# Optimization experiments

Measured on AMD Instinct MI355X. Metric: run time of the kernel, lower is better.

The kernel has to match this reference:

```python
import jax, jax.numpy as jnp
import numpy as np

DIM = 2048
NUM_HEADS = 8
HEAD_DIM = DIM // NUM_HEADS
BATCH = 16384
EPS = 1e-5


def setup_inputs() -> dict:
    key = jax.random.key(0)
    ks = jax.random.split(key, 10)
    s = 1.0 / np.sqrt(DIM)
    inp = {
        "x": jax.random.normal(ks[0], (BATCH, 1, DIM), dtype=jnp.float32),
        "w_q": jax.random.uniform(ks[1], (DIM, DIM), jnp.float32, -s, s),
        "b_q": jax.random.uniform(ks[2], (DIM,), jnp.float32, -s, s),
        "w_k": jax.random.uniform(ks[3], (DIM, DIM), jnp.float32, -s, s),
        "b_k": jax.random.uniform(ks[4], (DIM,), jnp.float32, -s, s),
        "w_v": jax.random.uniform(ks[5], (DIM, DIM), jnp.float32, -s, s),
        "b_v": jax.random.uniform(ks[6], (DIM,), jnp.float32, -s, s),
        "w_o": jax.random.uniform(ks[7], (DIM, DIM), jnp.float32, -s, s),
        "b_o": jax.random.uniform(ks[8], (DIM,), jnp.float32, -s, s),
        "ln_gamma": jnp.ones((DIM,), jnp.float32),
        "ln_beta": jnp.zeros((DIM,), jnp.float32),
    }
    return inp


def _layer_norm(x, gamma, beta):
    mean = jnp.mean(x, axis=-1, keepdims=True)
    var = jnp.mean(jnp.square(x - mean), axis=-1, keepdims=True)
    return (x - mean) * jax.lax.rsqrt(var + EPS) * gamma + beta


def reference(x, w_q, b_q, w_k, b_k, w_v, b_v, w_o, b_o, ln_gamma, ln_beta):
    # x: (B, 1, D). Dropout is identity (eval mode).
    residual = x
    h = _layer_norm(x, ln_gamma, ln_beta)
    q = h @ w_q.T + b_q  # (B, 1, D)
    k = h @ w_k.T + b_k
    v = h @ w_v.T + b_v
    B = x.shape[0]
    # (B, H, 1, hd)
    qh = q.reshape(B, 1, NUM_HEADS, HEAD_DIM).transpose(0, 2, 1, 3)
    kh = k.reshape(B, 1, NUM_HEADS, HEAD_DIM).transpose(0, 2, 1, 3)
    vh = v.reshape(B, 1, NUM_HEADS, HEAD_DIM).transpose(0, 2, 1, 3)
    scale = HEAD_DIM ** -0.5
    # (B, H, 1, 1); with seq_len=1 softmax is trivially 1, but keep the math faithful
    scores = jnp.einsum("bhqd,bhkd->bhqk", qh, kh) * scale
    probs = jax.nn.softmax(scores, axis=-1)
    attn = jnp.einsum("bhqk,bhkd->bhqd", probs, vh)  # (B, H, 1, hd)
    attn = attn.transpose(0, 2, 1, 3).reshape(B, 1, DIM)
    out = attn @ w_o.T + b_o
    out = out + residual
    return out[:, 0, :]  # squeeze seq dim -> (B, D)
```

## Files before the change

kernel.cpp:

```cpp
#include <hip/hip_runtime.h>
#include <hip/hip_bf16.h>
#include <cstdint>

#define D_MODEL 2048
#define N_BATCH 16384

typedef __attribute__((ext_vector_type(8))) __bf16 bf16x8;
typedef __attribute__((ext_vector_type(4))) float f32x4;

__device__ __forceinline__ unsigned short f2bf(float f) {
    unsigned int u = __builtin_bit_cast(unsigned int, f);
    u += 0x7fffu + ((u >> 16) & 1u);
    return (unsigned short)(u >> 16);
}

__global__ __launch_bounds__(256) void ln_kernel(
    const float* __restrict__ x, const float* __restrict__ gamma,
    const float* __restrict__ beta, unsigned short* __restrict__ h)
{
    const int row = blockIdx.x;
    const int t = threadIdx.x;
    const float4* x4 = reinterpret_cast<const float4*>(x + (long)row * D_MODEL);
    float4 a = x4[t];
    float4 b = x4[256 + t];
    float s  = a.x + a.y + a.z + a.w + b.x + b.y + b.z + b.w;
    float ss = a.x*a.x + a.y*a.y + a.z*a.z + a.w*a.w
             + b.x*b.x + b.y*b.y + b.z*b.z + b.w*b.w;
    #pragma unroll
    for (int off = 32; off; off >>= 1) {
        s  += __shfl_xor(s, off);
        ss += __shfl_xor(ss, off);
    }
    __shared__ float red[8];
    const int lane = t & 63, wid = t >> 6;
    if (lane == 0) { red[wid*2] = s; red[wid*2+1] = ss; }
    __syncthreads();
    s  = red[0] + red[2] + red[4] + red[6];
    ss = red[1] + red[3] + red[5] + red[7];
    const float mean = s * (1.0f / D_MODEL);
    const float var  = ss * (1.0f / D_MODEL) - mean * mean;
    const float inv  = rsqrtf(var + 1e-5f);

    const float4* g4  = reinterpret_cast<const float4*>(gamma);
    const float4* be4 = reinterpret_cast<const float4*>(beta);
    ushort4* h4 = reinterpret_cast<ushort4*>(h + (long)row * D_MODEL);
    {
        float4 g = g4[t], be = be4[t];
        ushort4 o;
        o.x = f2bf((a.x - mean) * inv * g.x + be.x);
        o.y = f2bf((a.y - mean) * inv * g.y + be.y);
        o.z = f2bf((a.z - mean) * inv * g.z + be.z);
        o.w = f2bf((a.w - mean) * inv * g.w + be.w);
        h4[t] = o;
    }
    {
        float4 g = g4[256 + t], be = be4[256 + t];
        ushort4 o;
        o.x = f2bf((b.x - mean) * inv * g.x + be.x);
        o.y = f2bf((b.y - mean) * inv * g.y + be.y);
        o.z = f2bf((b.z - mean) * inv * g.z + be.z);
        o.w = f2bf((b.w - mean) * inv * g.w + be.w);
        h4[256 + t] = o;
    }
}

__global__ __launch_bounds__(256) void transpose_f32_to_bf16(
    const float* __restrict__ in, unsigned short* __restrict__ out, int Dm)
{
    __shared__ float tile[32][33];
    const int nb = Dm >> 5;
    const int k0 = (blockIdx.x % nb) * 32;
    const int j0 = (blockIdx.x / nb) * 32;
    const int tx = threadIdx.x & 31, ty0 = threadIdx.x >> 5;
    #pragma unroll
    for (int i = 0; i < 32; i += 8) {
        int j = ty0 + i;
        tile[j][tx] = in[(long)(j0 + j) * Dm + k0 + tx];
    }
    __syncthreads();
    #pragma unroll
    for (int i = 0; i < 32; i += 8) {
        int kk = ty0 + i;
        out[(long)(k0 + kk) * Dm + j0 + tx] = f2bf(tile[tx][kk]);
    }
}

__global__ __launch_bounds__(256) void convert_bf16(
    const float* __restrict__ in, unsigned short* __restrict__ out, long n)
{
    long i = ((long)blockIdx.x * 256 + threadIdx.x) * 8;
    if (i >= n) return;
    const float4* in4 = reinterpret_cast<const float4*>(in + i);
    float4 a = in4[0], b = in4[1];
    union { unsigned short u[8]; uint4 v; } o;
    o.u[0] = f2bf(a.x); o.u[1] = f2bf(a.y); o.u[2] = f2bf(a.z); o.u[3] = f2bf(a.w);
    o.u[4] = f2bf(b.x); o.u[5] = f2bf(b.y); o.u[6] = f2bf(b.z); o.u[7] = f2bf(b.w);
    *reinterpret_cast<uint4*>(out + i) = o.v;
}

__global__ __launch_bounds__(256) void bias_combine(
    const float* __restrict__ w_o, const float* __restrict__ b_v,
    const float* __restrict__ b_o, float* __restrict__ b_c)
{
    const int n = blockIdx.x;
    const int t = threadIdx.x;
    const float4* w4 = reinterpret_cast<const float4*>(w_o + (long)n * D_MODEL);
    const float4* v4 = reinterpret_cast<const float4*>(b_v);
    float4 a = w4[t], b = w4[256 + t], va = v4[t], vb = v4[256 + t];
    float s = a.x*va.x + a.y*va.y + a.z*va.z + a.w*va.w
            + b.x*vb.x + b.y*vb.y + b.z*vb.z + b.w*vb.w;
    #pragma unroll
    for (int off = 32; off; off >>= 1) s += __shfl_xor(s, off);
    __shared__ float red[4];
    const int lane = t & 63, wid = t >> 6;
    if (lane == 0) red[wid] = s;
    __syncthreads();
    if (t == 0) b_c[n] = red[0] + red[1] + red[2] + red[3] + b_o[n];
}

__global__ __launch_bounds__(256, 2) void gemm_bt_128(
    const unsigned short* __restrict__ A, const unsigned short* __restrict__ B,
    unsigned short* __restrict__ C, int M, int N, int K)
{
    const int nBN = N >> 7;
    int wg = blockIdx.x;
    const int nwg = gridDim.x;
    const int cpx = nwg >> 3;
    wg = (wg & 7) * cpx + (wg >> 3);
    const int bm = wg / nBN, bn = wg % nBN;

    const int t = threadIdx.x;
    const int lane = t & 63, wid = t >> 6;
    const int wr = wid >> 1, wc = wid & 1;

    __shared__ __align__(16) unsigned short Alds[128 * 32];
    __shared__ __align__(16) unsigned short Blds[128 * 32];

    f32x4 acc[4][4];
    #pragma unroll
    for (int i = 0; i < 4; i++)
        #pragma unroll
        for (int j = 0; j < 4; j++) acc[i][j] = (f32x4){0.f, 0.f, 0.f, 0.f};

    const long Abase = (long)bm * 128 * K;
    const long Bbase = (long)bn * 128 * K;
    const int ci0 = wid * 64 + lane;
    const int ci1 = 256 + ci0;
    const int r0 = ci0 >> 2, c0 = (ci0 & 3) * 8;
    const int r1 = ci1 >> 2, c1 = (ci1 & 3) * 8;

    const int arow = wr * 64 + (lane & 15);
    const int brow = wc * 64 + (lane & 15);
    const int koff = (lane >> 4) * 8;

    for (int k0 = 0; k0 < K; k0 += 32) {
        __builtin_amdgcn_global_load_lds(
            (const __attribute__((address_space(1))) void*)(A + Abase + (long)r0 * K + k0 + c0),
            (__attribute__((address_space(3))) void*)(Alds + wid * 512), 16, 0, 0);
        __builtin_amdgcn_global_load_lds(
            (const __attribute__((address_space(1))) void*)(A + Abase + (long)r1 * K + k0 + c1),
            (__attribute__((address_space(3))) void*)(Alds + 2048 + wid * 512), 16, 0, 0);
        __builtin_amdgcn_global_load_lds(
            (const __attribute__((address_space(1))) void*)(B + Bbase + (long)r0 * K + k0 + c0),
            (__attribute__((address_space(3))) void*)(Blds + wid * 512), 16, 0, 0);
        __builtin_amdgcn_global_load_lds(
            (const __attribute__((address_space(1))) void*)(B + Bbase + (long)r1 * K + k0 + c1),
            (__attribute__((address_space(3))) void*)(Blds + 2048 + wid * 512), 16, 0, 0);
        __syncthreads();

        bf16x8 af[4], bfr[4];
        #pragma unroll
        for (int m = 0; m < 4; m++)
            af[m] = *reinterpret_cast<const bf16x8*>(&Alds[(arow + m * 16) * 32 + koff]);
        #pragma unroll
        for (int n = 0; n < 4; n++)
            bfr[n] = *reinterpret_cast<const bf16x8*>(&Blds[(brow + n * 16) * 32 + koff]);
        #pragma unroll
        for (int m = 0; m < 4; m++)
            #pragma unroll
            for (int n = 0; n < 4; n++)
                acc[m][n] = __builtin_amdgcn_mfma_f32_16x16x32_bf16(af[m], bfr[n], acc[m][n], 0, 0, 0);
        __syncthreads();
    }

    const int crow0 = bm * 128 + wr * 64 + ((lane >> 4) << 2);
    const int ccol0 = bn * 128 + wc * 64 + (lane & 15);
    #pragma unroll
    for (int m = 0; m < 4; m++)
        #pragma unroll
        for (int j = 0; j < 4; j++) {
            const long r = crow0 + m * 16 + j;
            #pragma unroll
            for (int n = 0; n < 4; n++)
                C[r * N + ccol0 + n * 16] = f2bf(acc[m][n][j]);
        }
}

__global__ __launch_bounds__(512, 2) void gemm_bt_256(
    const unsigned short* __restrict__ A, const unsigned short* __restrict__ B,
    float* __restrict__ C, const float* __restrict__ bias,
    const float* __restrict__ resid, int M, int N, int K)
{
    __shared__ __align__(16) char lds[131072];

    const int nBN = N >> 8;
    int wg = blockIdx.x;
    const int cpx = gridDim.x >> 3;
    wg = (wg & 7) * cpx + (wg >> 3);
    const int bm = wg / nBN, bn = wg % nBN;

    const int t = threadIdx.x;
    const int lane = t & 63, wid = t >> 6;
    const int wr = wid >> 2;
    const int wcn = wid & 3;

    const int r_lo = t >> 2, cch = t & 3;
    const int schunk = (cch ^ ((r_lo >> 2) & 3)) * 8;
    const unsigned short* sA0 = A + (long)(bm * 256 + r_lo) * K + schunk;
    const unsigned short* sA1 = sA0 + (long)128 * K;
    const unsigned short* sB0 = B + (long)(bn * 256 + r_lo) * K + schunk;
    const unsigned short* sB1 = sB0 + (long)128 * K;

#define STAGE_A(d) do { \
    __builtin_amdgcn_global_load_lds((const __attribute__((address_space(1))) void*)sA0, \
        (__attribute__((address_space(3))) void*)(lds + (d) * 32768 + wid * 1024), 16, 0, 0); \
    __builtin_amdgcn_global_load_lds((const __attribute__((address_space(1))) void*)sA1, \
        (__attribute__((address_space(3))) void*)(lds + (d) * 32768 + 8192 + wid * 1024), 16, 0, 0); \
    sA0 += 32; sA1 += 32; } while (0)
#define STAGE_B(d) do { \
    __builtin_amdgcn_global_load_lds((const __attribute__((address_space(1))) void*)sB0, \
        (__attribute__((address_space(3))) void*)(lds + (d) * 32768 + 16384 + wid * 1024), 16, 0, 0); \
    __builtin_amdgcn_global_load_lds((const __attribute__((address_space(1))) void*)sB1, \
        (__attribute__((address_space(3))) void*)(lds + (d) * 32768 + 24576 + wid * 1024), 16, 0, 0); \
    sB0 += 32; sB1 += 32; } while (0)

    const int l15 = lane & 15, l4 = lane >> 4;
    const int koffb = ((l4 ^ ((l15 >> 2) & 3)) << 4);
    const int aRowB = (wr * 128 + l15) * 64 + koffb;
    const int bRowB = 16384 + (wcn * 64 + l15) * 64 + koffb;

    f32x4 acc[8][4];
    #pragma unroll
    for (int i = 0; i < 8; i++)
        #pragma unroll
        for (int j = 0; j < 4; j++) acc[i][j] = (f32x4){0.f, 0.f, 0.f, 0.f};

    const int nt = K >> 5;
    STAGE_A(0); STAGE_B(0);
    STAGE_A(1); STAGE_B(1);
    STAGE_A(2); STAGE_B(2);

    for (int kt = 0; kt < nt; ++kt) {
        const int bufb = (kt & 3) * 32768;
        const int slack = nt - 1 - kt;
        if (slack >= 2)      asm volatile("s_waitcnt vmcnt(8)" ::: "memory");
        else if (slack == 1) asm volatile("s_waitcnt vmcnt(4)" ::: "memory");
        else                 asm volatile("s_waitcnt vmcnt(0)" ::: "memory");
        __builtin_amdgcn_s_barrier();
        __builtin_amdgcn_sched_barrier(0);

        bf16x8 af[4], bfr[4];
        #pragma unroll
        for (int n = 0; n < 4; n++)
            bfr[n] = *reinterpret_cast<const bf16x8*>(lds + bufb + bRowB + n * 1024);
        #pragma unroll
        for (int m = 0; m < 4; m++)
            af[m] = *reinterpret_cast<const bf16x8*>(lds + bufb + aRowB + m * 1024);
        if (kt + 3 < nt) STAGE_A((kt + 3) & 3);
        __builtin_amdgcn_s_setprio(1);
        #pragma unroll
        for (int m = 0; m < 4; m++)
            #pragma unroll
            for (int n = 0; n < 4; n++)
                acc[m][n] = __builtin_amdgcn_mfma_f32_16x16x32_bf16(af[m], bfr[n], acc[m][n], 0, 0, 0);
        __builtin_amdgcn_s_setprio(0);

        __builtin_amdgcn_s_barrier();
        __builtin_amdgcn_sched_barrier(0);

        #pragma unroll
        for (int m = 0; m < 4; m++)
            af[m] = *reinterpret_cast<const bf16x8*>(lds + bufb + aRowB + 4096 + m * 1024);
        if (kt + 3 < nt) STAGE_B((kt + 3) & 3);
        __builtin_amdgcn_s_setprio(1);
        #pragma unroll
        for (int m = 0; m < 4; m++)
            #pragma unroll
            for (int n = 0; n < 4; n++)
                acc[4 + m][n] = __builtin_amdgcn_mfma_f32_16x16x32_bf16(af[m], bfr[n], acc[4 + m][n], 0, 0, 0);
        __builtin_amdgcn_s_setprio(0);
    }
#undef STAGE_A
#undef STAGE_B

    const int crow0 = bm * 256 + wr * 128 + l4 * 4;
    const int ccol0 = bn * 256 + wcn * 64 + l15;
    #pragma unroll
    for (int m = 0; m < 8; m++)
        #pragma unroll
        for (int j = 0; j < 4; j++) {
            const long r = crow0 + m * 16 + j;
            float* crow = C + r * N;
            const float* rrow = resid + r * N;
            #pragma unroll
            for (int n = 0; n < 4; n++) {
                const int col = ccol0 + n * 16;
                crow[col] = acc[m][n][j] + bias[col] + rrow[col];
            }
        }
}

extern "C" void kernel_launch(void* const* d_in, const int* in_sizes, int n_in,
                              void* d_out, int out_size, void* d_ws, size_t ws_size,
                              hipStream_t stream) {
    const float* x     = (const float*)d_in[0];
    const float* w_v   = (const float*)d_in[5];
    const float* b_v   = (const float*)d_in[6];
    const float* w_o   = (const float*)d_in[7];
    const float* b_o   = (const float*)d_in[8];
    const float* gamma = (const float*)d_in[9];
    const float* beta  = (const float*)d_in[10];
    float* out = (float*)d_out;

    char* ws = (char*)d_ws;
    unsigned short* h   = (unsigned short*)(ws);
    unsigned short* wvT = (unsigned short*)(ws + 67108864L);
    unsigned short* woB = (unsigned short*)(ws + 67108864L + 8388608L);
    unsigned short* Wc  = (unsigned short*)(ws + 67108864L + 2 * 8388608L);
    float*          b_c = (float*)(ws + 67108864L + 3 * 8388608L);

    ln_kernel<<<N_BATCH, 256, 0, stream>>>(x, gamma, beta, h);
    transpose_f32_to_bf16<<<(D_MODEL / 32) * (D_MODEL / 32), 256, 0, stream>>>(w_v, wvT, D_MODEL);
    convert_bf16<<<(D_MODEL * (long)D_MODEL) / (256 * 8), 256, 0, stream>>>(w_o, woB, (long)D_MODEL * D_MODEL);
    bias_combine<<<D_MODEL, 256, 0, stream>>>(w_o, b_v, b_o, b_c);
    gemm_bt_128<<<(D_MODEL / 128) * (D_MODEL / 128), 256, 0, stream>>>(
        woB, wvT, Wc, D_MODEL, D_MODEL, D_MODEL);
    gemm_bt_256<<<(N_BATCH / 256) * (D_MODEL / 256), 512, 0, stream>>>(
        h, Wc, out, b_c, x, N_BATCH, D_MODEL, D_MODEL);
}
```

Baseline: 251.2 us.

## Shrink main GEMM tile to 256x128 with triple-buffered LDS for higher occupancy

The large GEMM now uses a 256x128 output tile per 512-thread block instead of 256x256. It keeps a 3-stage LDS ring of 24 KB per stage instead of 4 stages of 32 KB, and asks for 4 blocks per CU. The per-iteration split into two barrier-separated MFMA halves is replaced by one staged load and one 16-MFMA block, with an explicit lgkmcnt wait. This doubles the grid and raises occupancy, at the cost of halving per-block reuse of A and loading it twice as often from global memory, with a shallower prefetch depth.

After: 257.7 us. 1.03x slower.

```diff
diff --git a/kernel.cpp b/kernel.cpp
--- a/kernel.cpp
+++ b/kernel.cpp
@@ -196,14 +196,14 @@
         }
 }
 
-__global__ __launch_bounds__(512, 2) void gemm_bt_256(
+__global__ __launch_bounds__(512, 4) void gemm_bt_256(
     const unsigned short* __restrict__ A, const unsigned short* __restrict__ B,
     float* __restrict__ C, const float* __restrict__ bias,
     const float* __restrict__ resid, int M, int N, int K)
 {
-    __shared__ __align__(16) char lds[131072];
-
-    const int nBN = N >> 8;
+    __shared__ __align__(16) char lds[73728];
+
+    const int nBN = N >> 7;
     int wg = blockIdx.x;
     const int cpx = gridDim.x >> 3;
     wg = (wg & 7) * cpx + (wg >> 3);
@@ -211,54 +211,53 @@
 
     const int t = threadIdx.x;
     const int lane = t & 63, wid = t >> 6;
-    const int wr = wid >> 2;
-    const int wcn = wid & 3;
+    const int wr = wid >> 1;
+    const int wcn = wid & 1;
 
     const int r_lo = t >> 2, cch = t & 3;
-    const int schunk = (cch ^ ((r_lo >> 2) & 3)) * 8;
+    const int schunk = (cch ^ ((r_lo >> 1) & 3)) * 8;
     const unsigned short* sA0 = A + (long)(bm * 256 + r_lo) * K + schunk;
     const unsigned short* sA1 = sA0 + (long)128 * K;
-    const unsigned short* sB0 = B + (long)(bn * 256 + r_lo) * K + schunk;
-    const unsigned short* sB1 = sB0 + (long)128 * K;
-
-#define STAGE_A(d) do { \
+    const unsigned short* sB0 = B + (long)(bn * 128 + r_lo) * K + schunk;
+
+#define STAGE_AB(d) do { \
+    const int dst_ = (d) * 24576 + wid * 1024; \
     __builtin_amdgcn_global_load_lds((const __attribute__((address_space(1))) void*)sA0, \
-        (__attribute__((address_space(3))) void*)(lds + (d) * 32768 + wid * 1024), 16, 0, 0); \
+        (__attribute__((address_space(3))) void*)(lds + dst_), 16, 0, 0); \
     __builtin_amdgcn_global_load_lds((const __attribute__((address_space(1))) void*)sA1, \
-        (__attribute__((address_space(3))) void*)(lds + (d) * 32768 + 8192 + wid * 1024), 16, 0, 0); \
-    sA0 += 32; sA1 += 32; } while (0)
-#define STAGE_B(d) do { \
+        (__attribute__((address_space(3))) void*)(lds + dst_ + 8192), 16, 0, 0); \
     __builtin_amdgcn_global_load_lds((const __attribute__((address_space(1))) void*)sB0, \
-        (__attribute__((address_space(3))) void*)(lds + (d) * 32768 + 16384 + wid * 1024), 16, 0, 0); \
-    __builtin_amdgcn_global_load_lds((const __attribute__((address_space(1))) void*)sB1, \
-        (__attribute__((address_space(3))) void*)(lds + (d) * 32768 + 24576 + wid * 1024), 16, 0, 0); \
-    sB0 += 32; sB1 += 32; } while (0)
+        (__attribute__((address_space(3))) void*)(lds + dst_ + 16384), 16, 0, 0); \
+    sA0 += 32; sA1 += 32; sB0 += 32; } while (0)
 
     const int l15 = lane & 15, l4 = lane >> 4;
-    const int koffb = ((l4 ^ ((l15 >> 2) & 3)) << 4);
-    const int aRowB = (wr * 128 + l15) * 64 + koffb;
+    const int koffb = ((l4 ^ ((l15 >> 1) & 3)) << 4);
+    const int aRowB = (wr * 64 + l15) * 64 + koffb;
     const int bRowB = 16384 + (wcn * 64 + l15) * 64 + koffb;
 
-    f32x4 acc[8][4];
-    #pragma unroll
-    for (int i = 0; i < 8; i++)
+    f32x4 acc[4][4];
+    #pragma unroll
+    for (int i = 0; i < 4; i++)
         #pragma unroll
         for (int j = 0; j < 4; j++) acc[i][j] = (f32x4){0.f, 0.f, 0.f, 0.f};
 
     const int nt = K >> 5;
-    STAGE_A(0); STAGE_B(0);
-    STAGE_A(1); STAGE_B(1);
-    STAGE_A(2); STAGE_B(2);
-
+    STAGE_AB(0);
+    STAGE_AB(1);
+
+    int buf = 0;
     for (int kt = 0; kt < nt; ++kt) {
-        const int bufb = (kt & 3) * 32768;
-        const int slack = nt - 1 - kt;
-        if (slack >= 2)      asm volatile("s_waitcnt vmcnt(8)" ::: "memory");
-        else if (slack == 1) asm volatile("s_waitcnt vmcnt(4)" ::: "memory");
-        else                 asm volatile("s_waitcnt vmcnt(0)" ::: "memory");
+        if (kt < nt - 1) asm volatile("s_waitcnt vmcnt(3)" ::: "memory");
+        else             asm volatile("s_waitcnt vmcnt(0)" ::: "memory");
         __builtin_amdgcn_s_barrier();
         __builtin_amdgcn_sched_barrier(0);
 
+        if (kt + 2 < nt) {
+            const int nb2 = buf + 2 >= 3 ? buf - 1 : buf + 2;
+            STAGE_AB(nb2);
+        }
+
+        const int bufb = buf * 24576;
         bf16x8 af[4], bfr[4];
         #pragma unroll
         for (int n = 0; n < 4; n++)
@@ -266,7 +265,9 @@
         #pragma unroll
         for (int m = 0; m < 4; m++)
             af[m] = *reinterpret_cast<const bf16x8*>(lds + bufb + aRowB + m * 1024);
-        if (kt + 3 < nt) STAGE_A((kt + 3) & 3);
+
+        asm volatile("s_waitcnt lgkmcnt(0)" ::: "memory");
+        __builtin_amdgcn_sched_barrier(0);
         __builtin_amdgcn_s_setprio(1);
         #pragma unroll
         for (int m = 0; m < 4; m++)
@@ -275,28 +276,14 @@
                 acc[m][n] = __builtin_amdgcn_mfma_f32_16x16x32_bf16(af[m], bfr[n], acc[m][n], 0, 0, 0);
         __builtin_amdgcn_s_setprio(0);
 
-        __builtin_amdgcn_s_barrier();
-        __builtin_amdgcn_sched_barrier(0);
-
-        #pragma unroll
-        for (int m = 0; m < 4; m++)
-            af[m] = *reinterpret_cast<const bf16x8*>(lds + bufb + aRowB + 4096 + m * 1024);
-        if (kt + 3 < nt) STAGE_B((kt + 3) & 3);
-        __builtin_amdgcn_s_setprio(1);
-        #pragma unroll
-        for (int m = 0; m < 4; m++)
-            #pragma unroll
-            for (int n = 0; n < 4; n++)
-                acc[4 + m][n] = __builtin_amdgcn_mfma_f32_16x16x32_bf16(af[m], bfr[n], acc[4 + m][n], 0, 0, 0);
-        __builtin_amdgcn_s_setprio(0);
-    }
-#undef STAGE_A
-#undef STAGE_B
-
-    const int crow0 = bm * 256 + wr * 128 + l4 * 4;
-    const int ccol0 = bn * 256 + wcn * 64 + l15;
-    #pragma unroll
-    for (int m = 0; m < 8; m++)
+        buf = (buf + 1 == 3) ? 0 : buf + 1;
+    }
+#undef STAGE_AB
+
+    const int crow0 = bm * 256 + wr * 64 + l4 * 4;
+    const int ccol0 = bn * 128 + wcn * 64 + l15;
+    #pragma unroll
+    for (int m = 0; m < 4; m++)
         #pragma unroll
         for (int j = 0; j < 4; j++) {
             const long r = crow0 + m * 16 + j;
@@ -335,6 +322,6 @@
     bias_combine<<<D_MODEL, 256, 0, stream>>>(w_o, b_v, b_o, b_c);
     gemm_bt_128<<<(D_MODEL / 128) * (D_MODEL / 128), 256, 0, stream>>>(
         woB, wvT, Wc, D_MODEL, D_MODEL, D_MODEL);
-    gemm_bt_256<<<(N_BATCH / 256) * (D_MODEL / 256), 512, 0, stream>>>(
+    gemm_bt_256<<<(N_BATCH / 256) * (D_MODEL / 128), 512, 0, stream>>>(
         h, Wc, out, b_c, x, N_BATCH, D_MODEL, D_MODEL);
 }
```
